# Kernel tuning notes

Measured on AMD Instinct MI355X. Metric: run time of the kernel, lower is better.

The kernel has to match this reference:

```python
import jax, jax.numpy as jnp
import numpy as np

H = 32  # hidden_layer_size

def setup_inputs() -> dict:
    key = jax.random.key(0)
    ks = jax.random.split(key, 12)
    B, T, I = 4096, 512, 1
    x = jax.random.normal(ks[0], (B, T, I), dtype=jnp.float32)
    # linear_1: input_size -> H
    W1 = jax.random.normal(ks[1], (H, I), dtype=jnp.float32) * (1.0 / np.sqrt(I))
    b1 = jnp.zeros((H,), dtype=jnp.float32)
    # LSTM layer 0 (input H) and layer 1 (input H); torch gate order i,f,g,o
    Wih0 = jax.random.normal(ks[2], (4 * H, H), dtype=jnp.float32) * np.sqrt(2.0 / H)  # kaiming
    Whh0 = jax.random.normal(ks[3], (4 * H, H), dtype=jnp.float32) * (1.0 / np.sqrt(H))
    bih0 = jnp.zeros((4 * H,), dtype=jnp.float32)
    bhh0 = jnp.zeros((4 * H,), dtype=jnp.float32)
    Wih1 = jax.random.normal(ks[4], (4 * H, H), dtype=jnp.float32) * np.sqrt(2.0 / H)
    Whh1 = jax.random.normal(ks[5], (4 * H, H), dtype=jnp.float32) * (1.0 / np.sqrt(H))
    bih1 = jnp.zeros((4 * H,), dtype=jnp.float32)
    bhh1 = jnp.zeros((4 * H,), dtype=jnp.float32)
    # linear_2: num_layers*H -> 1
    W2 = jax.random.normal(ks[6], (1, 2 * H), dtype=jnp.float32) * (1.0 / np.sqrt(2 * H))
    b2 = jnp.zeros((1,), dtype=jnp.float32)
    return {"x": x, "W1": W1, "b1": b1,
            "Wih0": Wih0, "Whh0": Whh0, "bih0": bih0, "bhh0": bhh0,
            "Wih1": Wih1, "Whh1": Whh1, "bih1": bih1, "bhh1": bhh1,
            "W2": W2, "b2": b2}


def _lstm_layer(inp, Wih, Whh, bih, bhh):
    # inp: [B, T, H_in]; returns (ys [B, T, H], h_final [B, H])
    B = inp.shape[0]
    # precompute input-to-gate projections for all timesteps (one big GEMM)
    pre = jnp.einsum('bti,gi->tbg', inp, Wih) + (bih + bhh)  # [T, B, 4H]

    def step(carry, p_t):
        h, c = carry
        z = p_t + h @ Whh.T  # [B, 4H]
        i, f, g, o = jnp.split(z, 4, axis=-1)
        i = jax.nn.sigmoid(i)
        f = jax.nn.sigmoid(f)
        g = jnp.tanh(g)
        o = jax.nn.sigmoid(o)
        c = f * c + i * g
        h = o * jnp.tanh(c)
        return (h, c), h

    h0 = jnp.zeros((B, H), dtype=inp.dtype)
    c0 = jnp.zeros((B, H), dtype=inp.dtype)
    (h_f, _), ys = jax.lax.scan(step, (h0, c0), pre)
    return jnp.transpose(ys, (1, 0, 2)), h_f


def reference(x, W1, b1, Wih0, Whh0, bih0, bhh0, Wih1, Whh1, bih1, bhh1, W2, b2):
    # linear_1 + ReLU
    h = jax.nn.relu(jnp.einsum('bti,oi->bto', x, W1) + b1)  # [B, T, H]
    y0, hf0 = _lstm_layer(h, Wih0, Whh0, bih0, bhh0)
    _, hf1 = _lstm_layer(y0, Wih1, Whh1, bih1, bhh1)
    # h_n.permute(1,0,2).reshape(B, -1) -> concat layer finals along feature dim
    hcat = jnp.concatenate([hf0, hf1], axis=-1)  # [B, 2H]
    # dropout: eval mode (identity)
    preds = hcat @ W2.T + b2  # [B, 1]
    return preds[:, -1]  # [B]
```

## Files before the change

kernel.cpp:

```cpp
#include <hip/hip_runtime.h>

#define HH 32
#define NB 16
#define NT 1024
#define TT 512

typedef float f32x4 __attribute__((ext_vector_type(4)));
typedef __bf16 bf16x8 __attribute__((ext_vector_type(8)));
typedef unsigned int u32;
typedef unsigned short u16;
typedef u32 u32x4 __attribute__((ext_vector_type(4)));

#if __has_builtin(__builtin_amdgcn_exp2f)
#define EXP2F(x) __builtin_amdgcn_exp2f(x)
#else
#define EXP2F(x) exp2f(x)
#endif
#if __has_builtin(__builtin_amdgcn_rcpf)
#define RCPF(x) __builtin_amdgcn_rcpf(x)
#else
#define RCPF(x) (1.0f / (x))
#endif

#define S_SIGM (-1.44269504f)
#define S_TANH (-2.88539008f)

static __device__ __forceinline__ f32x4 mfma16(bf16x8 a, bf16x8 b, f32x4 c) {
  return __builtin_amdgcn_mfma_f32_16x16x32_bf16(a, b, c, 0, 0, 0);
}

static __device__ __forceinline__ u32 rne_hi(u32 b) {
  return (b + 0x7FFFu + ((b >> 16) & 1u)) & 0xFFFF0000u;
}
static __device__ __forceinline__ u32 pack_hi16(u32 a, u32 b) {
#if __has_builtin(__builtin_amdgcn_perm)
  return __builtin_amdgcn_perm(a, b, 0x03020706u);
#else
  return (b & 0xFFFF0000u) | (a >> 16);
#endif
}


static __device__ __forceinline__ bf16x8 load_wfrag_hi(const float* __restrict__ M,
                                                       int tile, int lane) {
  const int m = lane & 15;
  const int q = m & 3;
  const int gi = q * HH + 4 * tile + (m >> 2);
  const int kappa = lane >> 4;
  const float s = (q == 2) ? S_TANH : S_SIGM;
  u32 r[8];
#pragma unroll
  for (int e = 0; e < 8; ++e) {
    const float v = M[gi * HH + 8 * kappa + 4 * (e & 1) + (e >> 1)] * s;
    r[e] = rne_hi(__builtin_bit_cast(u32, v));
  }
  u32x4 hw;
#pragma unroll
  for (int i = 0; i < 4; ++i) hw[i] = pack_hi16(r[2 * i], r[2 * i + 1]);
  return __builtin_bit_cast(bf16x8, hw);
}

static __device__ __forceinline__ void store_h(u16* hiA, u16* loA, int fw, float h) {
  const u32 b = __builtin_bit_cast(u32, h);
  const u32 r = rne_hi(b);
  hiA[fw] = (u16)(r >> 16);
  const float lof = h - __builtin_bit_cast(float, r);
  loA[fw] = (u16)(__builtin_bit_cast(u32, lof) >> 16);
}

__global__ void __launch_bounds__(NT)
lstm_fused_v5(const float* __restrict__ x,
              const float* __restrict__ W1, const float* __restrict__ b1,
              const float* __restrict__ Wih0, const float* __restrict__ Whh0,
              const float* __restrict__ bih0, const float* __restrict__ bhh0,
              const float* __restrict__ Wih1, const float* __restrict__ Whh1,
              const float* __restrict__ bih1, const float* __restrict__ bhh1,
              const float* __restrict__ W2, const float* __restrict__ b2,
              float* __restrict__ out, int T)
{
  __shared__ __align__(16) u16 h0hi[2][NB * HH], h0lo[2][NB * HH];
  __shared__ __align__(16) u16 h1hi[2][NB * HH], h1lo[2][NB * HH];
  __shared__ __align__(16) u16 hxhi[2][NB * HH], hxlo[2][NB * HH];
  __shared__ __align__(16) float xT[TT * NB];

  const int tid  = threadIdx.x;
  const int lane = tid & 63;
  const int wS   = __builtin_amdgcn_readfirstlane(tid >> 6);
  const bool isL0 = (wS < 8);
  const int tau  = wS & 7;
  const int G    = lane >> 4;
  const int b0   = blockIdx.x * NB;

  const float* Wr   = isL0 ? Whh0 : Whh1;
  const float* Wi_  = isL0 ? Wih0 : Wih1;
  const float* bihp = isL0 ? bih0 : bih1;
  const float* bhhp = isL0 ? bhh0 : bhh1;

  const bf16x8 wr = load_wfrag_hi(Wr,  tau, lane);
  const bf16x8 wi = load_wfrag_hi(Wi_, tau, lane);

  const int uu = 4 * tau + G;
  const int bq = lane & 15;
  f32x4 bias;
#pragma unroll
  for (int q = 0; q < 4; ++q) {
    const float s = (q == 2) ? S_TANH : S_SIGM;
    bias[q] = (bihp[q * HH + uu] + bhhp[q * HH + uu]) * s;
  }
  const int fw  = (bq + 16 * (uu >> 3)) * 8 + 2 * (uu & 3) + ((uu >> 2) & 1);
  const int frd = lane * 8;

  const float W1u = W1[uu], b1u = b1[uu];
  const float W2v = W2[(isL0 ? 0 : HH) + uu];

  {
    const int row = tid & 15;
    const int c0i = (tid >> 4) * 8;
    if (c0i + 8 <= T) {
      const float* xp = x + (size_t)(b0 + row) * T + c0i;
      const float4 v0 = *(const float4*)(xp);
      const float4 v1 = *(const float4*)(xp + 4);
      xT[(c0i + 0) * NB + row] = v0.x;
      xT[(c0i + 1) * NB + row] = v0.y;
      xT[(c0i + 2) * NB + row] = v0.z;
      xT[(c0i + 3) * NB + row] = v0.w;
      xT[(c0i + 4) * NB + row] = v1.x;
      xT[(c0i + 5) * NB + row] = v1.y;
      xT[(c0i + 6) * NB + row] = v1.z;
      xT[(c0i + 7) * NB + row] = v1.w;
    }
  }
  if (tid < 512) {
    ((u32*)h0hi)[tid] = 0; ((u32*)h0lo)[tid] = 0;
    ((u32*)h1hi)[tid] = 0; ((u32*)h1lo)[tid] = 0;
    ((u32*)hxhi)[tid] = 0; ((u32*)hxlo)[tid] = 0;
  }
  __syncthreads();
  if (isL0) {
    const float hv = fmaxf(__builtin_fmaf(x[(size_t)(b0 + bq) * T], W1u, b1u), 0.0f);
    store_h(hxhi[0], hxlo[0], fw, hv);
  }
  float cS = 0.0f, hS = 0.0f;
  __syncthreads();

#define GATES(z)                                                        \
    { const float ei = EXP2F(z[0]), ef = EXP2F(z[1]);                   \
      const float eg = EXP2F(z[2]), eo = EXP2F(z[3]);                   \
      const float iv = RCPF(1.0f + ei), fv = RCPF(1.0f + ef);           \
      const float gv = __builtin_fmaf(2.0f, RCPF(1.0f + eg), -1.0f);    \
      const float ov = RCPF(1.0f + eo);                                 \
      cS = __builtin_fmaf(fv, cS, iv * gv);                             \
      const float th = __builtin_fmaf(2.0f,                             \
          RCPF(1.0f + EXP2F(cS * S_TANH)), -1.0f);                      \
      hS = ov * th; }

#define STEP(kk, WB, DO_L0, DO_L1, DO_HIN)                              \
  {                                                                     \
    const int RB = (WB) ^ 1;                                            \
    if (isL0) {                                                         \
      if (DO_L0) {                                                      \
        const bf16x8 shi = *(const bf16x8*)&h0hi[RB][frd];              \
        const bf16x8 slo = *(const bf16x8*)&h0lo[RB][frd];              \
        const bf16x8 phi = *(const bf16x8*)&hxhi[WB][frd];              \
        const bf16x8 plo = *(const bf16x8*)&hxlo[WB][frd];              \
        f32x4 z = mfma16(wi, plo, bias);                                \
        z = mfma16(wi, phi, z);                                         \
        z = mfma16(wr, slo, z);                                         \
        z = mfma16(wr, shi, z);                                         \
        if (DO_HIN) {                                                   \
          const float xv = xT[((kk) + 1) * NB + bq];                    \
          const float hv = fmaxf(__builtin_fmaf(xv, W1u, b1u), 0.0f);   \
          store_h(hxhi[RB], hxlo[RB], fw, hv);                          \
        }                                                               \
        GATES(z);                                                       \
        store_h(h0hi[WB], h0lo[WB], fw, hS);                            \
      }                                                                 \
    } else {                                                            \
      if (DO_L1) {                                                      \
        const bf16x8 shi = *(const bf16x8*)&h1hi[WB][frd];              \
        const bf16x8 slo = *(const bf16x8*)&h1lo[WB][frd];              \
        const bf16x8 phi = *(const bf16x8*)&h0hi[RB][frd];              \
        const bf16x8 plo = *(const bf16x8*)&h0lo[RB][frd];              \
        f32x4 z = mfma16(wi, plo, bias);                                \
        z = mfma16(wi, phi, z);                                         \
        z = mfma16(wr, slo, z);                                         \
        z = mfma16(wr, shi, z);                                         \
        GATES(z);                                                       \
        store_h(h1hi[RB], h1lo[RB], fw, hS);                            \
      }                                                                 \
    }                                                                   \
    __syncthreads();                                                    \
  }

  STEP(0, 0, true, false, true);
  for (int kk = 1; kk + 1 < T; kk += 2) {
    STEP(kk, 1, true, true, true);
    STEP(kk + 1, 0, true, true, true);
  }
  STEP(T - 1, 1, true, true, false);
  STEP(T, 0, false, true, false);

#undef STEP
#undef GATES

  xT[((isL0 ? 0 : HH) + uu) * NB + bq] = hS * W2v;
  __syncthreads();
  if (tid < NB) {
    float acc = b2[0];
#pragma unroll
    for (int j = 0; j < 2 * HH; ++j) acc += xT[j * NB + tid];
    out[b0 + tid] = acc;
  }
}

extern "C" void kernel_launch(void* const* d_in, const int* in_sizes, int n_in,
                              void* d_out, int out_size, void* d_ws, size_t ws_size,
                              hipStream_t stream) {
  const float* x    = (const float*)d_in[0];
  const float* W1   = (const float*)d_in[1];
  const float* b1   = (const float*)d_in[2];
  const float* Wih0 = (const float*)d_in[3];
  const float* Whh0 = (const float*)d_in[4];
  const float* bih0 = (const float*)d_in[5];
  const float* bhh0 = (const float*)d_in[6];
  const float* Wih1 = (const float*)d_in[7];
  const float* Whh1 = (const float*)d_in[8];
  const float* bih1 = (const float*)d_in[9];
  const float* bhh1 = (const float*)d_in[10];
  const float* W2   = (const float*)d_in[11];
  const float* b2   = (const float*)d_in[12];

  const int B = out_size;
  const int I = in_sizes[1] / HH;
  const int T = in_sizes[0] / (B * I);
  const int blocks = B / NB;

  lstm_fused_v5<<<blocks, NT, 0, stream>>>(
      x, W1, b1, Wih0, Whh0, bih0, bhh0, Wih1, Whh1, bih1, bhh1, W2, b2,
      (float*)d_out, T);
}
```

Baseline: 233.4 us.

## Halve block size with two gate tiles per wave and packed hi/lo h layout

Cuts the block from 16 to 8 waves. Each wave now computes two hidden-unit tiles (A and B), which doubles the MFMA and gate work per wave and gives two independent accumulation chains. The hidden state is stored as packed hi/lo bf16 pairs in u32 slots, and the weight fragments are duplicated so the hi and lo products come out of one K=32 MFMA. The aim is cheaper per-step barriers and more instruction-level parallelism. In exchange it raises register pressure and changes occupancy per CU.

```diff
diff --git a/kernel.cpp b/kernel.cpp
--- a/kernel.cpp
+++ b/kernel.cpp
@@ -2,7 +2,7 @@
 
 #define HH 32
 #define NB 16
-#define NT 1024
+#define NT 512
 #define TT 512
 
 typedef float f32x4 __attribute__((ext_vector_type(4)));
@@ -39,37 +39,33 @@
   return (b & 0xFFFF0000u) | (a >> 16);
 #endif
 }
-
-
-static __device__ __forceinline__ bf16x8 load_wfrag_hi(const float* __restrict__ M,
-                                                       int tile, int lane) {
+static __device__ __forceinline__ u32 pack_hl(float h) {
+  const u32 b = __builtin_bit_cast(u32, h);
+  const u32 r = rne_hi(b);
+  const float lo = h - __builtin_bit_cast(float, r);
+  return pack_hi16(r, __builtin_bit_cast(u32, lo));
+}
+
+static __device__ __forceinline__ bf16x8 load_wfrag_ph(const float* __restrict__ M,
+                                                       int tile, int half, int lane) {
   const int m = lane & 15;
   const int q = m & 3;
   const int gi = q * HH + 4 * tile + (m >> 2);
   const int kappa = lane >> 4;
   const float s = (q == 2) ? S_TANH : S_SIGM;
-  u32 r[8];
-#pragma unroll
-  for (int e = 0; e < 8; ++e) {
-    const float v = M[gi * HH + 8 * kappa + 4 * (e & 1) + (e >> 1)] * s;
-    r[e] = rne_hi(__builtin_bit_cast(u32, v));
-  }
+  const float* p = M + gi * HH + 16 * half + 4 * kappa;
   u32x4 hw;
 #pragma unroll
-  for (int i = 0; i < 4; ++i) hw[i] = pack_hi16(r[2 * i], r[2 * i + 1]);
+  for (int i = 0; i < 4; ++i) {
+    const float v = p[i] * s;
+    const u32 w16 = rne_hi(__builtin_bit_cast(u32, v)) >> 16;
+    hw[i] = w16 | (w16 << 16);
+  }
   return __builtin_bit_cast(bf16x8, hw);
 }
 
-static __device__ __forceinline__ void store_h(u16* hiA, u16* loA, int fw, float h) {
-  const u32 b = __builtin_bit_cast(u32, h);
-  const u32 r = rne_hi(b);
-  hiA[fw] = (u16)(r >> 16);
-  const float lof = h - __builtin_bit_cast(float, r);
-  loA[fw] = (u16)(__builtin_bit_cast(u32, lof) >> 16);
-}
-
 __global__ void __launch_bounds__(NT)
-lstm_fused_v5(const float* __restrict__ x,
+lstm_fused_v6(const float* __restrict__ x,
               const float* __restrict__ W1, const float* __restrict__ b1,
               const float* __restrict__ Wih0, const float* __restrict__ Whh0,
               const float* __restrict__ bih0, const float* __restrict__ bhh0,
@@ -78,17 +74,18 @@
               const float* __restrict__ W2, const float* __restrict__ b2,
               float* __restrict__ out, int T)
 {
-  __shared__ __align__(16) u16 h0hi[2][NB * HH], h0lo[2][NB * HH];
-  __shared__ __align__(16) u16 h1hi[2][NB * HH], h1lo[2][NB * HH];
-  __shared__ __align__(16) u16 hxhi[2][NB * HH], hxlo[2][NB * HH];
+  __shared__ __align__(16) u32 h0P[2][2][256];
+  __shared__ __align__(16) u32 h1P[2][2][256];
+  __shared__ __align__(16) u32 hxP[2][2][256];
   __shared__ __align__(16) float xT[TT * NB];
 
   const int tid  = threadIdx.x;
   const int lane = tid & 63;
   const int wS   = __builtin_amdgcn_readfirstlane(tid >> 6);
-  const bool isL0 = (wS < 8);
-  const int tau  = wS & 7;
-  const int G    = lane >> 4;
+  const bool isL0 = (wS < 4);
+  const int tq   = wS & 3;
+  const int kap  = lane >> 4;
+  const int b    = lane & 15;
   const int b0   = blockIdx.x * NB;
 
   const float* Wr   = isL0 ? Whh0 : Whh1;
@@ -96,97 +93,111 @@
   const float* bihp = isL0 ? bih0 : bih1;
   const float* bhhp = isL0 ? bhh0 : bhh1;
 
-  const bf16x8 wr = load_wfrag_hi(Wr,  tau, lane);
-  const bf16x8 wi = load_wfrag_hi(Wi_, tau, lane);
-
-  const int uu = 4 * tau + G;
-  const int bq = lane & 15;
-  f32x4 bias;
+  const bf16x8 wrA0 = load_wfrag_ph(Wr,  tq,     0, lane);
+  const bf16x8 wrA1 = load_wfrag_ph(Wr,  tq,     1, lane);
+  const bf16x8 wiA0 = load_wfrag_ph(Wi_, tq,     0, lane);
+  const bf16x8 wiA1 = load_wfrag_ph(Wi_, tq,     1, lane);
+  const bf16x8 wrB0 = load_wfrag_ph(Wr,  tq + 4, 0, lane);
+  const bf16x8 wrB1 = load_wfrag_ph(Wr,  tq + 4, 1, lane);
+  const bf16x8 wiB0 = load_wfrag_ph(Wi_, tq + 4, 0, lane);
+  const bf16x8 wiB1 = load_wfrag_ph(Wi_, tq + 4, 1, lane);
+
+  const int uA = 4 * tq + kap;
+  const int uB = uA + 16;
+  f32x4 biasA, biasB;
 #pragma unroll
   for (int q = 0; q < 4; ++q) {
     const float s = (q == 2) ? S_TANH : S_SIGM;
-    bias[q] = (bihp[q * HH + uu] + bhhp[q * HH + uu]) * s;
-  }
-  const int fw  = (bq + 16 * (uu >> 3)) * 8 + 2 * (uu & 3) + ((uu >> 2) & 1);
-  const int frd = lane * 8;
-
-  const float W1u = W1[uu], b1u = b1[uu];
-  const float W2v = W2[(isL0 ? 0 : HH) + uu];
+    biasA[q] = (bihp[q * HH + uA] + bhhp[q * HH + uA]) * s;
+    biasB[q] = (bihp[q * HH + uB] + bhhp[q * HH + uB]) * s;
+  }
+  const int slot = tq * 64 + b * 4 + kap;
+  const int frd  = lane * 8;
+
+  const float W1a = W1[uA], b1a = b1[uA];
+  const float W1b = W1[uB], b1b = b1[uB];
+  const int   w2o = isL0 ? 0 : HH;
+  const float W2a = W2[w2o + uA], W2b = W2[w2o + uB];
 
   {
-    const int row = tid & 15;
-    const int c0i = (tid >> 4) * 8;
-    if (c0i + 8 <= T) {
-      const float* xp = x + (size_t)(b0 + row) * T + c0i;
-      const float4 v0 = *(const float4*)(xp);
-      const float4 v1 = *(const float4*)(xp + 4);
-      xT[(c0i + 0) * NB + row] = v0.x;
-      xT[(c0i + 1) * NB + row] = v0.y;
-      xT[(c0i + 2) * NB + row] = v0.z;
-      xT[(c0i + 3) * NB + row] = v0.w;
-      xT[(c0i + 4) * NB + row] = v1.x;
-      xT[(c0i + 5) * NB + row] = v1.y;
-      xT[(c0i + 6) * NB + row] = v1.z;
-      xT[(c0i + 7) * NB + row] = v1.w;
+    const int row  = tid & 15;
+    const int cbase = (tid >> 4) * 16;
+    if (cbase + 16 <= T) {
+      const float* xp = x + (size_t)(b0 + row) * T + cbase;
+#pragma unroll
+      for (int j = 0; j < 16; j += 4) {
+        const float4 v = *(const float4*)(xp + j);
+        xT[(cbase + j + 0) * NB + row] = v.x;
+        xT[(cbase + j + 1) * NB + row] = v.y;
+        xT[(cbase + j + 2) * NB + row] = v.z;
+        xT[(cbase + j + 3) * NB + row] = v.w;
+      }
     }
   }
-  if (tid < 512) {
-    ((u32*)h0hi)[tid] = 0; ((u32*)h0lo)[tid] = 0;
-    ((u32*)h1hi)[tid] = 0; ((u32*)h1lo)[tid] = 0;
-    ((u32*)hxhi)[tid] = 0; ((u32*)hxlo)[tid] = 0;
-  }
+  ((u32*)h0P)[tid] = 0; ((u32*)h0P)[tid + 512] = 0;
+  ((u32*)h1P)[tid] = 0; ((u32*)h1P)[tid + 512] = 0;
+  ((u32*)hxP)[tid] = 0; ((u32*)hxP)[tid + 512] = 0;
   __syncthreads();
+
   if (isL0) {
-    const float hv = fmaxf(__builtin_fmaf(x[(size_t)(b0 + bq) * T], W1u, b1u), 0.0f);
-    store_h(hxhi[0], hxlo[0], fw, hv);
-  }
-  float cS = 0.0f, hS = 0.0f;
+    const float xv = xT[b];
+    hxP[0][0][slot] = pack_hl(fmaxf(__builtin_fmaf(xv, W1a, b1a), 0.0f));
+    hxP[0][1][slot] = pack_hl(fmaxf(__builtin_fmaf(xv, W1b, b1b), 0.0f));
+  }
+  float cA = 0.0f, cB = 0.0f, hA = 0.0f, hB = 0.0f;
   __syncthreads();
 
-#define GATES(z)                                                        \
-    { const float ei = EXP2F(z[0]), ef = EXP2F(z[1]);                   \
-      const float eg = EXP2F(z[2]), eo = EXP2F(z[3]);                   \
-      const float iv = RCPF(1.0f + ei), fv = RCPF(1.0f + ef);           \
-      const float gv = __builtin_fmaf(2.0f, RCPF(1.0f + eg), -1.0f);    \
-      const float ov = RCPF(1.0f + eo);                                 \
-      cS = __builtin_fmaf(fv, cS, iv * gv);                             \
-      const float th = __builtin_fmaf(2.0f,                             \
-          RCPF(1.0f + EXP2F(cS * S_TANH)), -1.0f);                      \
-      hS = ov * th; }
+#define GATES(z, c, h) {                                                \
+    const float ei = EXP2F(z[0]), ef = EXP2F(z[1]);                     \
+    const float eg = EXP2F(z[2]), eo = EXP2F(z[3]);                     \
+    const float iv = RCPF(1.0f + ei), fv = RCPF(1.0f + ef);             \
+    const float gv = __builtin_fmaf(2.0f, RCPF(1.0f + eg), -1.0f);      \
+    const float ov = RCPF(1.0f + eo);                                   \
+    c = __builtin_fmaf(fv, c, iv * gv);                                 \
+    h = ov * __builtin_fmaf(2.0f, RCPF(1.0f + EXP2F(c * S_TANH)), -1.0f); \
+  }
 
 #define STEP(kk, WB, DO_L0, DO_L1, DO_HIN)                              \
   {                                                                     \
     const int RB = (WB) ^ 1;                                            \
     if (isL0) {                                                         \
       if (DO_L0) {                                                      \
-        const bf16x8 shi = *(const bf16x8*)&h0hi[RB][frd];              \
-        const bf16x8 slo = *(const bf16x8*)&h0lo[RB][frd];              \
-        const bf16x8 phi = *(const bf16x8*)&hxhi[WB][frd];              \
-        const bf16x8 plo = *(const bf16x8*)&hxlo[WB][frd];              \
-        f32x4 z = mfma16(wi, plo, bias);                                \
-        z = mfma16(wi, phi, z);                                         \
-        z = mfma16(wr, slo, z);                                         \
-        z = mfma16(wr, shi, z);                                         \
+        const bf16x8 S0 = *(const bf16x8*)((const u16*)h0P[RB][0] + frd); \
+        const bf16x8 S1 = *(const bf16x8*)((const u16*)h0P[RB][1] + frd); \
+        const bf16x8 P0 = *(const bf16x8*)((const u16*)hxP[WB][0] + frd); \
+        const bf16x8 P1 = *(const bf16x8*)((const u16*)hxP[WB][1] + frd); \
+        f32x4 zA = mfma16(wiA1, P1, biasA);                             \
+        f32x4 zB = mfma16(wiB1, P1, biasB);                             \
+        zA = mfma16(wiA0, P0, zA);  zB = mfma16(wiB0, P0, zB);          \
+        zA = mfma16(wrA1, S1, zA);  zB = mfma16(wrB1, S1, zB);          \
+        zA = mfma16(wrA0, S0, zA);  zB = mfma16(wrB0, S0, zB);          \
         if (DO_HIN) {                                                   \
-          const float xv = xT[((kk) + 1) * NB + bq];                    \
-          const float hv = fmaxf(__builtin_fmaf(xv, W1u, b1u), 0.0f);   \
-          store_h(hxhi[RB], hxlo[RB], fw, hv);                          \
+          const float xv = xT[((kk) + 1) * NB + b];                     \
+          hxP[RB][0][slot] =                                            \
+              pack_hl(fmaxf(__builtin_fmaf(xv, W1a, b1a), 0.0f));       \
+          hxP[RB][1][slot] =                                            \
+              pack_hl(fmaxf(__builtin_fmaf(xv, W1b, b1b), 0.0f));       \
         }                                                               \
-        GATES(z);                                                       \
-        store_h(h0hi[WB], h0lo[WB], fw, hS);                            \
+        GATES(zA, cA, hA);                                              \
+        GATES(zB, cB, hB);                                              \
+        h0P[WB][0][slot] = pack_hl(hA);                                 \
+        h0P[WB][1][slot] = pack_hl(hB);                                 \
       }                                                                 \
     } else {                                                            \
       if (DO_L1) {                                                      \
-        const bf16x8 shi = *(const bf16x8*)&h1hi[WB][frd];              \
-        const bf16x8 slo = *(const bf16x8*)&h1lo[WB][frd];              \
-        const bf16x8 phi = *(const bf16x8*)&h0hi[RB][frd];              \
-        const bf16x8 plo = *(const bf16x8*)&h0lo[RB][frd];              \
-        f32x4 z = mfma16(wi, plo, bias);                                \
-        z = mfma16(wi, phi, z);                                         \
-        z = mfma16(wr, slo, z);                                         \
-        z = mfma16(wr, shi, z);                                         \
-        GATES(z);                                                       \
-        store_h(h1hi[RB], h1lo[RB], fw, hS);                            \
+        const bf16x8 S0 = *(const bf16x8*)((const u16*)h1P[WB][0] + frd); \
+        const bf16x8 S1 = *(const bf16x8*)((const u16*)h1P[WB][1] + frd); \
+        const bf16x8 P0 = *(const bf16x8*)((const u16*)h0P[RB][0] + frd); \
+        const bf16x8 P1 = *(const bf16x8*)((const u16*)h0P[RB][1] + frd); \
+        f32x4 zA = mfma16(wiA1, P1, biasA);                             \
+        f32x4 zB = mfma16(wiB1, P1, biasB);                             \
+        zA = mfma16(wiA0, P0, zA);  zB = mfma16(wiB0, P0, zB);          \
+        zA = mfma16(wrA1, S1, zA);  zB = mfma16(wrB1, S1, zB);          \
+        zA = mfma16(wrA0, S0, zA);  zB = mfma16(wrB0, S0, zB);          \
+        GATES(zA, cA, hA);                                              \
+        GATES(zB, cB, hB);                                              \
+        h1P[RB][0][slot] = pack_hl(hA);                                 \
+        h1P[RB][1][slot] = pack_hl(hB);                                 \
       }                                                                 \
     }                                                                   \
     __syncthreads();                                                    \
@@ -203,12 +214,12 @@
 #undef STEP
 #undef GATES
 
-  xT[((isL0 ? 0 : HH) + uu) * NB + bq] = hS * W2v;
+  xT[(wS * 4 + kap) * NB + b] = __builtin_fmaf(hA, W2a, hB * W2b);
   __syncthreads();
   if (tid < NB) {
     float acc = b2[0];
 #pragma unroll
-    for (int j = 0; j < 2 * HH; ++j) acc += xT[j * NB + tid];
+    for (int j = 0; j < 32; ++j) acc += xT[j * NB + tid];
     out[b0 + tid] = acc;
   }
 }
@@ -235,7 +246,7 @@
   const int T = in_sizes[0] / (B * I);
   const int blocks = B / NB;
 
-  lstm_fused_v5<<<blocks, NT, 0, stream>>>(
+  lstm_fused_v6<<<blocks, NT, 0, stream>>>(
       x, W1, b1, Wih0, Whh0, bih0, bhh0, Wih1, Whh1, bih1, bhh1, W2, b2,
       (float*)d_out, T);
 }
```

Result: no change. 232.4 us (-0.4%).
